# Optimization experiments

Hardware: AMD Instinct MI355X
Metric: run time of the kernel (lower is better)

Reference implementation:

```python
import jax, jax.numpy as jnp
import numpy as np

N_NODES = 100000
N_EDGES = 3200000
IN_DIM, HID_DIM, OUT_DIM = 128, 128, 64
NUM_LAYERS = 5


def setup_inputs() -> dict:
    key = jax.random.key(0)
    ks = jax.random.split(key, 2 + 2 * NUM_LAYERS)
    h = jax.random.normal(ks[0], (N_NODES, IN_DIM), dtype=jnp.float32)
    edge_index = jax.random.randint(ks[1], (2, N_EDGES), 0, N_NODES, dtype=jnp.int64)
    dims = [IN_DIM] + [HID_DIM] * (NUM_LAYERS - 1) + [OUT_DIM]
    inp = {"h": h, "edge_index": edge_index}
    for i in range(NUM_LAYERS):
        fan_in = dims[i]
        bound = 1.0 / np.sqrt(fan_in)
        inp[f"W{i}"] = jax.random.uniform(ks[2 + 2 * i], (dims[i], dims[i + 1]), jnp.float32, -bound, bound)
        inp[f"b{i}"] = jax.random.uniform(ks[3 + 2 * i], (dims[i + 1],), jnp.float32, -bound, bound)
    return inp


def _gin_layer(h, src, dst, W, b):
    # sum aggregation: agg[v] = sum_{(u->v) in E} h[u]
    agg = jax.ops.segment_sum(h[src], dst, num_segments=N_NODES)
    # eps = 0, learn_eps = False: rst = (1 + 0) * h + agg, then MLP (single Linear)
    return (h + agg) @ W + b


def reference(h, edge_index, W0, b0, W1, b1, W2, b2, W3, b3, W4, b4):
    src, dst = edge_index[0], edge_index[1]
    Ws = [W0, W1, W2, W3, W4]
    bs = [b0, b1, b2, b3, b4]
    for i in range(NUM_LAYERS):
        h = _gin_layer(h, src, dst, Ws[i], bs[i])
    return h
```

## Files before the change

kernel.cpp:

```cpp
#include <hip/hip_runtime.h>

#define N_NODES 100000
#define N_EDGES 3200000
#define NB 782
#define BCAP 5120
#define CHUNK_EDGES 4096
#define NCHUNKS ((N_EDGES + CHUNK_EDGES - 1) / CHUNK_EDGES)

typedef unsigned int uint;
typedef __attribute__((ext_vector_type(2))) uint u2v;
typedef __attribute__((ext_vector_type(4))) uint u4v;
typedef __attribute__((ext_vector_type(2))) float f2v;
typedef __attribute__((ext_vector_type(4))) float f4v;
typedef __attribute__((ext_vector_type(8))) short s8v;
typedef __attribute__((ext_vector_type(4))) float f32x4;


__global__ void detect_fmt(const uint* __restrict__ e, int* __restrict__ flag,
                           int* __restrict__ row_ptr) {
    if (threadIdx.x == 0) {
        *flag = (e[1] == 0u && e[3] == 0u && e[5] == 0u && e[7] == 0u) ? 1 : 0;
        row_ptr[N_NODES] = N_EDGES;
    }
}

__device__ __forceinline__ int load_idx(const void* edges, int fmt, long long i) {
    return fmt ? (int)((const long long*)edges)[i] : ((const int*)edges)[i];
}

__global__ __launch_bounds__(256) void part_hist(const void* __restrict__ edges,
                                                 const int* __restrict__ flag,
                                                 int* __restrict__ hist2,
                                                 int* __restrict__ bcount) {
    __shared__ int cnt[NB];
    for (int i = threadIdx.x; i < NB; i += 256) cnt[i] = 0;
    __syncthreads();
    int fmt = *flag;
    int c = blockIdx.x;
    int beg = c * CHUNK_EDGES, end = min(beg + CHUNK_EDGES, N_EDGES);
    for (int i = beg + threadIdx.x; i < end; i += 256) {
        int dst = load_idx(edges, fmt, (long long)N_EDGES + i);
        atomicAdd(&cnt[dst >> 7], 1);
    }
    __syncthreads();
    for (int i = threadIdx.x; i < NB; i += 256) {
        hist2[i * NCHUNKS + c] = cnt[i];
        if (cnt[i]) atomicAdd(&bcount[i], cnt[i]);
    }
}

__global__ void scan_kernel(const int* __restrict__ count, int* __restrict__ off_out, int n) {
    __shared__ int sums[1024];
    int t = threadIdx.x;
    int chunk = (n + 1023) >> 10;
    int beg = t * chunk;
    int end = min(beg + chunk, n);
    int s = 0;
    for (int i = beg; i < end; ++i) s += count[i];
    sums[t] = s;
    __syncthreads();
    int val = s;
    for (int off = 1; off < 1024; off <<= 1) {
        int other = (t >= off) ? sums[t - off] : 0;
        __syncthreads();
        val += other;
        sums[t] = val;
        __syncthreads();
    }
    int run = val - s;
    for (int i = beg; i < end; ++i) {
        off_out[i] = run;
        run += count[i];
    }
    if (end >= n) off_out[n] = run;
}

__global__ __launch_bounds__(1024) void chunk_scan(const int* __restrict__ hist2,
                                                   const int* __restrict__ boff,
                                                   int* __restrict__ base2) {
    __shared__ int s[1024];
    int b = blockIdx.x;
    int t = threadIdx.x;
    int v = (t < NCHUNKS) ? hist2[b * NCHUNKS + t] : 0;
    s[t] = v;
    __syncthreads();
    int val = v;
    for (int off = 1; off < 1024; off <<= 1) {
        int o = (t >= off) ? s[t - off] : 0;
        __syncthreads();
        val += o;
        s[t] = val;
        __syncthreads();
    }
    if (t < NCHUNKS) base2[t * NB + b] = boff[b] + val - v;
}

__global__ __launch_bounds__(256) void part_scatter(const void* __restrict__ edges,
                                                    const int* __restrict__ flag,
                                                    const int* __restrict__ base2,
                                                    uint* __restrict__ tmp) {
    __shared__ int cur[NB];
    int c = blockIdx.x;
    for (int i = threadIdx.x; i < NB; i += 256) cur[i] = base2[c * NB + i];
    __syncthreads();
    int fmt = *flag;
    int beg = c * CHUNK_EDGES, end = min(beg + CHUNK_EDGES, N_EDGES);
    for (int i = beg + threadIdx.x; i < end; i += 256) {
        int src = load_idx(edges, fmt, i);
        int dst = load_idx(edges, fmt, (long long)N_EDGES + i);
        int b = dst >> 7;
        int pos = atomicAdd(&cur[b], 1);
        tmp[pos] = ((uint)(dst & 127) << 17) | (uint)src;
    }
}

__global__ __launch_bounds__(256) void bucket_finalize(const uint* __restrict__ tmp,
                                                       const int* __restrict__ boff,
                                                       int* __restrict__ row_ptr,
                                                       int* __restrict__ esorted) {
    __shared__ uint s1[BCAP];
    __shared__ int s2[BCAP];
    __shared__ int cnt[128], pref[128], cur[128];
    int b = blockIdx.x;
    int beg = boff[b];
    int n = boff[b + 1] - beg;
    if (n > BCAP) n = BCAP;
    int t = threadIdx.x;
    if (t < 128) cnt[t] = 0;
    __syncthreads();
    for (int e = t; e < n; e += 256) {
        uint k = tmp[beg + e];
        s1[e] = k;
        atomicAdd(&cnt[k >> 17], 1);
    }
    __syncthreads();
    if (t < 128) pref[t] = cnt[t];
    __syncthreads();
    for (int off = 1; off < 128; off <<= 1) {
        int v = (t < 128 && t >= off) ? pref[t - off] : 0;
        __syncthreads();
        if (t < 128) pref[t] += v;
        __syncthreads();
    }
    if (t < 128) {
        int ex = pref[t] - cnt[t];
        cur[t] = ex;
        int node = b * 128 + t;
        if (node < N_NODES) row_ptr[node] = beg + ex;
    }
    __syncthreads();
    for (int e = t; e < n; e += 256) {
        uint k = s1[e];
        int p = atomicAdd(&cur[k >> 17], 1);
        s2[p] = (int)(k & 0x1FFFF);
    }
    __syncthreads();
    for (int e = t; e < n; e += 256) esorted[beg + e] = s2[e];
}


__device__ __forceinline__ uint bf16pack(float a, float b) {
    uint ua = __float_as_uint(a);
    ua = (ua + 0x7FFFu + ((ua >> 16) & 1u)) >> 16;
    uint ub = __float_as_uint(b);
    ub = (ub + 0x7FFFu + ((ub >> 16) & 1u)) >> 16;
    return ua | (ub << 16);
}
__device__ __forceinline__ float bf_lo(uint u) { return __uint_as_float(u << 16); }
__device__ __forceinline__ float bf_hi(uint u) { return __uint_as_float(u & 0xFFFF0000u); }


__global__ __launch_bounds__(256) void matstage(const float* __restrict__ Wl,
                                                const float* __restrict__ bl,
                                                const float* __restrict__ Sin,
                                                float* __restrict__ Sout,
                                                float* __restrict__ cout) {
    __shared__ float S[128 * 64];
    int tid = threadIdx.x;
    int b = blockIdx.x;
    for (int i = tid; i < 128 * 16; i += 256) ((f4v*)S)[i] = ((const f4v*)Sin)[i];
    __syncthreads();
    if (b < 32) {
        int rr = tid >> 6;
        int c = tid & 63;
        int r = b * 4 + rr;
        const float* wrow = &Wl[r * 128];
        float s = 0.f;
#pragma unroll 8
        for (int k = 0; k < 128; ++k) s += wrow[k] * S[k * 64 + c];
        Sout[r * 64 + c] = s;
    } else if (tid < 64) {
        float s = 0.f;
        for (int k = 0; k < 128; ++k) s += bl[k] * S[k * 64 + tid];
        cout[tid] = s;
    }
}

__global__ __launch_bounds__(256) void prep_z(const float* __restrict__ S0,
                                              const float* __restrict__ b4,
                                              u4v* __restrict__ Wt,
                                              float* __restrict__ c_all) {
    int idx = blockIdx.x * 256 + threadIdx.x;
    if (blockIdx.x == 0 && threadIdx.x < 64) c_all[4 * 64 + threadIdx.x] = b4[threadIdx.x];
    if (idx >= 64 * 16) return;
    int n = idx >> 4, c16 = idx & 15;
    u4v o;
#pragma unroll
    for (int q = 0; q < 4; ++q)
        o[q] = bf16pack(S0[(size_t)(c16 * 8 + 2 * q) * 64 + n],
                        S0[(size_t)(c16 * 8 + 2 * q + 1) * 64 + n]);
    Wt[n * 16 + (c16 ^ (n & 7))] = o;
}


__global__ __launch_bounds__(256) void agg64_step(const uint* __restrict__ z,
                                                  const int* __restrict__ row_ptr,
                                                  const int* __restrict__ esrc,
                                                  const float* __restrict__ cvec,
                                                  uint* __restrict__ zn) {
    const u2v* z2 = (const u2v*)z;
    int lane = threadIdx.x & 63;
    int c = lane & 15;
    int g = lane >> 4;
    int wid = (blockIdx.x * blockDim.x + threadIdx.x) >> 6;
    int nw = (gridDim.x * blockDim.x) >> 6;
    f4v cc = ((const f4v*)cvec)[c];
    for (int v = wid; v < N_NODES; v += nw) {
        f2v aX = {0.f, 0.f}, aY = {0.f, 0.f};
        int beg = row_ptr[v], end = row_ptr[v + 1];
        int i = beg;
        for (; i + 16 <= end; i += 16) {
            uint k[4];
            u2v u[4];
#pragma unroll
            for (int j = 0; j < 4; ++j) k[j] = (uint)esrc[i + 4 * j + g];
#pragma unroll
            for (int j = 0; j < 4; ++j) u[j] = z2[k[j] * 16u + (uint)c];
#pragma unroll
            for (int j = 0; j < 4; ++j) {
                f2v t0 = {bf_lo(u[j].x), bf_hi(u[j].x)};
                f2v t1 = {bf_lo(u[j].y), bf_hi(u[j].y)};
                aX += t0;
                aY += t1;
            }
        }
        for (; i < end; i += 4) {
            int idx = i + g;
            u2v uu = {0u, 0u};
            if (idx < end) uu = z2[(uint)esrc[idx] * 16u + (uint)c];
            f2v t0 = {bf_lo(uu.x), bf_hi(uu.x)};
            f2v t1 = {bf_lo(uu.y), bf_hi(uu.y)};
            aX += t0;
            aY += t1;
        }
        aX.x += __shfl_xor(aX.x, 16);
        aX.y += __shfl_xor(aX.y, 16);
        aY.x += __shfl_xor(aY.x, 16);
        aY.y += __shfl_xor(aY.y, 16);
        aX.x += __shfl_xor(aX.x, 32);
        aX.y += __shfl_xor(aX.y, 32);
        aY.x += __shfl_xor(aY.x, 32);
        aY.y += __shfl_xor(aY.y, 32);
        if (g == 0) {
            u2v self = z2[(uint)v * 16u + (uint)c];
            u2v o = {bf16pack(aX.x + bf_lo(self.x) + cc.x, aX.y + bf_hi(self.x) + cc.y),
                     bf16pack(aY.x + bf_lo(self.y) + cc.z, aY.y + bf_hi(self.y) + cc.w)};
            __builtin_nontemporal_store(o, &((u2v*)zn)[(uint)v * 16u + (uint)c]);
        }
    }
}

__global__ __launch_bounds__(256) void agg64_last(const uint* __restrict__ z,
                                                  const int* __restrict__ row_ptr,
                                                  const int* __restrict__ esrc,
                                                  const float* __restrict__ cvec,
                                                  float* __restrict__ out) {
    const u2v* z2 = (const u2v*)z;
    int lane = threadIdx.x & 63;
    int c = lane & 15;
    int g = lane >> 4;
    int wid = (blockIdx.x * blockDim.x + threadIdx.x) >> 6;
    int nw = (gridDim.x * blockDim.x) >> 6;
    f4v cc = ((const f4v*)cvec)[c];
    for (int v = wid; v < N_NODES; v += nw) {
        f2v aX = {0.f, 0.f}, aY = {0.f, 0.f};
        int beg = row_ptr[v], end = row_ptr[v + 1];
        int i = beg;
        for (; i + 16 <= end; i += 16) {
            uint k[4];
            u2v u[4];
#pragma unroll
            for (int j = 0; j < 4; ++j) k[j] = (uint)esrc[i + 4 * j + g];
#pragma unroll
            for (int j = 0; j < 4; ++j) u[j] = z2[k[j] * 16u + (uint)c];
#pragma unroll
            for (int j = 0; j < 4; ++j) {
                f2v t0 = {bf_lo(u[j].x), bf_hi(u[j].x)};
                f2v t1 = {bf_lo(u[j].y), bf_hi(u[j].y)};
                aX += t0;
                aY += t1;
            }
        }
        for (; i < end; i += 4) {
            int idx = i + g;
            u2v uu = {0u, 0u};
            if (idx < end) uu = z2[(uint)esrc[idx] * 16u + (uint)c];
            f2v t0 = {bf_lo(uu.x), bf_hi(uu.x)};
            f2v t1 = {bf_lo(uu.y), bf_hi(uu.y)};
            aX += t0;
            aY += t1;
        }
        aX.x += __shfl_xor(aX.x, 16);
        aX.y += __shfl_xor(aX.y, 16);
        aY.x += __shfl_xor(aY.x, 16);
        aY.y += __shfl_xor(aY.y, 16);
        aX.x += __shfl_xor(aX.x, 32);
        aX.y += __shfl_xor(aX.y, 32);
        aY.x += __shfl_xor(aY.x, 32);
        aY.y += __shfl_xor(aY.y, 32);
        if (g == 0) {
            u2v self = z2[(uint)v * 16u + (uint)c];
            f4v o = {aX.x + bf_lo(self.x) + cc.x, aX.y + bf_hi(self.x) + cc.y,
                     aY.x + bf_lo(self.y) + cc.z, aY.y + bf_hi(self.y) + cc.w};
            __builtin_nontemporal_store(o, &((f4v*)out)[(uint)v * 16u + (uint)c]);
        }
    }
}


__global__ __launch_bounds__(256) void mfma_gemm64(const float* __restrict__ x,
                                                   const u4v* __restrict__ Wt,
                                                   uint* __restrict__ y) {
    constexpr int SMEM = 32768 + 64 * 256;
    __shared__ char raw[SMEM];
    u4v* Asm = (u4v*)raw;
    u4v* Bsm = (u4v*)(raw + 32768);
    float* Cst = (float*)raw;
    int tid = threadIdx.x;
    int m0 = blockIdx.x * 128;

#pragma unroll
    for (int i = 0; i < 8; ++i) {
        int idx = tid + i * 256;
        int r = idx >> 4, c16 = idx & 15;
        int m = m0 + r;
        if (m >= N_NODES) m = N_NODES - 1;
        const float* src = &x[(size_t)m * 128 + c16 * 8];
        f4v v0 = *(const f4v*)src;
        f4v v1 = *(const f4v*)(src + 4);
        u4v o = {bf16pack(v0.x, v0.y), bf16pack(v0.z, v0.w),
                 bf16pack(v1.x, v1.y), bf16pack(v1.z, v1.w)};
        Asm[r * 16 + (c16 ^ (r & 7))] = o;
    }
#pragma unroll
    for (int i = 0; i < 4; ++i) Bsm[tid + i * 256] = Wt[tid + i * 256];
    __syncthreads();

    int lane = tid & 63;
    int w = tid >> 6;
    int n0w = w * 16;
    int lhi = lane >> 4, llo = lane & 15;
    f32x4 acc[8];
#pragma unroll
    for (int i = 0; i < 8; ++i) acc[i] = (f32x4){0.f, 0.f, 0.f, 0.f};

#pragma unroll
    for (int ks = 0; ks < 4; ++ks) {
        int cb = ks * 4 + lhi;
        int col = n0w + llo;
        u4v tb = Bsm[col * 16 + (cb ^ (col & 7))];
        s8v bfr = *(s8v*)&tb;
#pragma unroll
        for (int i = 0; i < 8; ++i) {
            int row = i * 16 + llo;
            u4v t = Asm[row * 16 + (cb ^ (row & 7))];
            s8v aa = *(s8v*)&t;
            acc[i] = __builtin_amdgcn_mfma_f32_16x16x32_bf16(aa, bfr, acc[i], 0, 0, 0);
        }
    }
    __syncthreads();
#pragma unroll
    for (int i = 0; i < 8; ++i)
#pragma unroll
        for (int r = 0; r < 4; ++r)
            Cst[(i * 16 + lhi * 4 + r) * 64 + n0w + llo] = acc[i][r];
    __syncthreads();
#pragma unroll
    for (int i = 0; i < 16; ++i) {
        int idx = tid + i * 256;
        int m = idx >> 5, np = idx & 31;
        if (m0 + m < N_NODES)
            y[(size_t)(m0 + m) * 32 + np] =
                bf16pack(Cst[m * 64 + 2 * np], Cst[m * 64 + 2 * np + 1]);
    }
}

extern "C" void kernel_launch(void* const* d_in, const int* in_sizes, int n_in,
                              void* d_out, int out_size, void* d_ws, size_t ws_size,
                              hipStream_t stream) {
    const float* h_in = (const float*)d_in[0];
    const void* edges = d_in[1];
    const float* W[5] = {(const float*)d_in[2], (const float*)d_in[4], (const float*)d_in[6],
                         (const float*)d_in[8], (const float*)d_in[10]};
    const float* B[5] = {(const float*)d_in[3], (const float*)d_in[5], (const float*)d_in[7],
                         (const float*)d_in[9], (const float*)d_in[11]};

    size_t off = 0;
    auto alloc = [&](size_t bytes) {
        void* p = (char*)d_ws + off;
        off = (off + bytes + 255) & ~(size_t)255;
        return p;
    };
    int* esorted = (int*)alloc((size_t)N_EDGES * 4);
    int* row_ptr = (int*)alloc((size_t)(N_NODES + 1) * 4);
    int* hist2 = (int*)alloc((size_t)NCHUNKS * NB * 4);
    int* base2 = (int*)alloc((size_t)NCHUNKS * NB * 4);
    int* bcount = (int*)alloc((size_t)NB * 4);
    int* boff = (int*)alloc((size_t)(NB + 1) * 4);
    int* flag = (int*)alloc(256);
    float* Sa = (float*)alloc(128 * 64 * 4);
    float* Sb = (float*)alloc(128 * 64 * 4);
    float* c_all = (float*)alloc(5 * 64 * 4);
    u4v* Wt_z = (u4v*)alloc((size_t)64 * 16 * 16);
    uint* zA = (uint*)alloc((size_t)N_NODES * 32 * 4);
    uint* zB = (uint*)alloc((size_t)N_NODES * 32 * 4);
    uint* tmp = (uint*)alloc((size_t)N_EDGES * 4);

    detect_fmt<<<1, 64, 0, stream>>>((const uint*)edges, flag, row_ptr);
    (void)hipMemsetAsync(bcount, 0, (size_t)NB * 4, stream);
    part_hist<<<NCHUNKS, 256, 0, stream>>>(edges, flag, hist2, bcount);
    scan_kernel<<<1, 1024, 0, stream>>>(bcount, boff, NB);
    chunk_scan<<<NB, 1024, 0, stream>>>(hist2, boff, base2);
    part_scatter<<<NCHUNKS, 256, 0, stream>>>(edges, flag, base2, tmp);
    bucket_finalize<<<NB, 256, 0, stream>>>(tmp, boff, row_ptr, esorted);

    matstage<<<33, 256, 0, stream>>>(W[3], B[3], W[4], Sa, c_all + 3 * 64);
    matstage<<<33, 256, 0, stream>>>(W[2], B[2], Sa, Sb, c_all + 2 * 64);
    matstage<<<33, 256, 0, stream>>>(W[1], B[1], Sb, Sa, c_all + 1 * 64);
    matstage<<<33, 256, 0, stream>>>(W[0], B[0], Sa, Sb, c_all + 0 * 64);
    prep_z<<<4, 256, 0, stream>>>(Sb, B[4], Wt_z, c_all);

    mfma_gemm64<<<(N_NODES + 127) / 128, 256, 0, stream>>>(h_in, Wt_z, zA);
    agg64_step<<<2048, 256, 0, stream>>>(zA, row_ptr, esorted, c_all + 0 * 64, zB);
    agg64_step<<<2048, 256, 0, stream>>>(zB, row_ptr, esorted, c_all + 1 * 64, zA);
    agg64_step<<<2048, 256, 0, stream>>>(zA, row_ptr, esorted, c_all + 2 * 64, zB);
    agg64_step<<<2048, 256, 0, stream>>>(zB, row_ptr, esorted, c_all + 3 * 64, zA);
    agg64_last<<<2048, 256, 0, stream>>>(zA, row_ptr, esorted, c_all + 4 * 64,
                                         (float*)d_out);
}
```

Baseline: 438.2 us.

## Widen aggregation loads to 16B per lane and coarsen edge scatter chunks

The aggregation kernels now have each lane load 16 bytes (8 bf16 values) per neighbor row, so 8 lanes cover a row and 8 edges are gathered in parallel per wavefront instead of 4. This is meant to cut the number of gather instructions and raise bytes in flight per request. Separately, part_scatter now runs 1024-thread blocks over 32768-edge chunks and reuses the base offsets of every eighth 4096-edge chunk, giving fewer blocks with larger per-block work. The scatter change relies on the 8-chunk grouping lining up with the histogram layout, and the wider per-node edge step may leave more lanes idle on low-degree nodes.

```diff
diff --git a/kernel.cpp b/kernel.cpp
--- a/kernel.cpp
+++ b/kernel.cpp
@@ -6,6 +6,8 @@
 #define BCAP 5120
 #define CHUNK_EDGES 4096
 #define NCHUNKS ((N_EDGES + CHUNK_EDGES - 1) / CHUNK_EDGES)
+#define CHUNK_S 32768
+#define NCHUNKS_S ((N_EDGES + CHUNK_S - 1) / CHUNK_S)
 
 typedef unsigned int uint;
 typedef __attribute__((ext_vector_type(2))) uint u2v;
@@ -95,17 +97,17 @@
     if (t < NCHUNKS) base2[t * NB + b] = boff[b] + val - v;
 }
 
-__global__ __launch_bounds__(256) void part_scatter(const void* __restrict__ edges,
-                                                    const int* __restrict__ flag,
-                                                    const int* __restrict__ base2,
-                                                    uint* __restrict__ tmp) {
+__global__ __launch_bounds__(1024) void part_scatter(const void* __restrict__ edges,
+                                                     const int* __restrict__ flag,
+                                                     const int* __restrict__ base2,
+                                                     uint* __restrict__ tmp) {
     __shared__ int cur[NB];
     int c = blockIdx.x;
-    for (int i = threadIdx.x; i < NB; i += 256) cur[i] = base2[c * NB + i];
+    for (int i = threadIdx.x; i < NB; i += 1024) cur[i] = base2[(c * 8) * NB + i];
     __syncthreads();
     int fmt = *flag;
-    int beg = c * CHUNK_EDGES, end = min(beg + CHUNK_EDGES, N_EDGES);
-    for (int i = beg + threadIdx.x; i < end; i += 256) {
+    int beg = c * CHUNK_S, end = min(beg + CHUNK_S, N_EDGES);
+    for (int i = beg + (int)threadIdx.x; i < end; i += 1024) {
         int src = load_idx(edges, fmt, i);
         int dst = load_idx(edges, fmt, (long long)N_EDGES + i);
         int b = dst >> 7;
@@ -218,54 +220,68 @@
                                                   const int* __restrict__ esrc,
                                                   const float* __restrict__ cvec,
                                                   uint* __restrict__ zn) {
-    const u2v* z2 = (const u2v*)z;
+    const u4v* z4 = (const u4v*)z;
     int lane = threadIdx.x & 63;
-    int c = lane & 15;
-    int g = lane >> 4;
+    int c = lane & 7;
+    int g = lane >> 3;
     int wid = (blockIdx.x * blockDim.x + threadIdx.x) >> 6;
     int nw = (gridDim.x * blockDim.x) >> 6;
-    f4v cc = ((const f4v*)cvec)[c];
+    f4v cc0 = ((const f4v*)cvec)[2 * c];
+    f4v cc1 = ((const f4v*)cvec)[2 * c + 1];
     for (int v = wid; v < N_NODES; v += nw) {
-        f2v aX = {0.f, 0.f}, aY = {0.f, 0.f};
+        f2v a0 = {0.f, 0.f}, a1 = {0.f, 0.f}, a2 = {0.f, 0.f}, a3 = {0.f, 0.f};
         int beg = row_ptr[v], end = row_ptr[v + 1];
         int i = beg;
-        for (; i + 16 <= end; i += 16) {
+        for (; i + 32 <= end; i += 32) {
             uint k[4];
-            u2v u[4];
-#pragma unroll
-            for (int j = 0; j < 4; ++j) k[j] = (uint)esrc[i + 4 * j + g];
-#pragma unroll
-            for (int j = 0; j < 4; ++j) u[j] = z2[k[j] * 16u + (uint)c];
+            u4v u[4];
+#pragma unroll
+            for (int j = 0; j < 4; ++j) k[j] = (uint)esrc[i + 8 * j + g];
+#pragma unroll
+            for (int j = 0; j < 4; ++j) u[j] = z4[k[j] * 8u + (uint)c];
 #pragma unroll
             for (int j = 0; j < 4; ++j) {
                 f2v t0 = {bf_lo(u[j].x), bf_hi(u[j].x)};
                 f2v t1 = {bf_lo(u[j].y), bf_hi(u[j].y)};
-                aX += t0;
-                aY += t1;
+                f2v t2 = {bf_lo(u[j].z), bf_hi(u[j].z)};
+                f2v t3 = {bf_lo(u[j].w), bf_hi(u[j].w)};
+                a0 += t0;
+                a1 += t1;
+                a2 += t2;
+                a3 += t3;
             }
         }
-        for (; i < end; i += 4) {
+        for (; i < end; i += 8) {
             int idx = i + g;
-            u2v uu = {0u, 0u};
-            if (idx < end) uu = z2[(uint)esrc[idx] * 16u + (uint)c];
+            u4v uu = {0u, 0u, 0u, 0u};
+            if (idx < end) uu = z4[(uint)esrc[idx] * 8u + (uint)c];
             f2v t0 = {bf_lo(uu.x), bf_hi(uu.x)};
             f2v t1 = {bf_lo(uu.y), bf_hi(uu.y)};
-            aX += t0;
-            aY += t1;
-        }
-        aX.x += __shfl_xor(aX.x, 16);
-        aX.y += __shfl_xor(aX.y, 16);
-        aY.x += __shfl_xor(aY.x, 16);
-        aY.y += __shfl_xor(aY.y, 16);
-        aX.x += __shfl_xor(aX.x, 32);
-        aX.y += __shfl_xor(aX.y, 32);
-        aY.x += __shfl_xor(aY.x, 32);
-        aY.y += __shfl_xor(aY.y, 32);
+            f2v t2 = {bf_lo(uu.z), bf_hi(uu.z)};
+            f2v t3 = {bf_lo(uu.w), bf_hi(uu.w)};
+            a0 += t0;
+            a1 += t1;
+            a2 += t2;
+            a3 += t3;
+        }
+#pragma unroll
+        for (int d = 8; d <= 32; d <<= 1) {
+            a0.x += __shfl_xor(a0.x, d);
+            a0.y += __shfl_xor(a0.y, d);
+            a1.x += __shfl_xor(a1.x, d);
+            a1.y += __shfl_xor(a1.y, d);
+            a2.x += __shfl_xor(a2.x, d);
+            a2.y += __shfl_xor(a2.y, d);
+            a3.x += __shfl_xor(a3.x, d);
+            a3.y += __shfl_xor(a3.y, d);
+        }
         if (g == 0) {
-            u2v self = z2[(uint)v * 16u + (uint)c];
-            u2v o = {bf16pack(aX.x + bf_lo(self.x) + cc.x, aX.y + bf_hi(self.x) + cc.y),
-                     bf16pack(aY.x + bf_lo(self.y) + cc.z, aY.y + bf_hi(self.y) + cc.w)};
-            __builtin_nontemporal_store(o, &((u2v*)zn)[(uint)v * 16u + (uint)c]);
+            u4v self = z4[(uint)v * 8u + (uint)c];
+            u4v o = {bf16pack(a0.x + bf_lo(self.x) + cc0.x, a0.y + bf_hi(self.x) + cc0.y),
+                     bf16pack(a1.x + bf_lo(self.y) + cc0.z, a1.y + bf_hi(self.y) + cc0.w),
+                     bf16pack(a2.x + bf_lo(self.z) + cc1.x, a2.y + bf_hi(self.z) + cc1.y),
+                     bf16pack(a3.x + bf_lo(self.w) + cc1.z, a3.y + bf_hi(self.w) + cc1.w)};
+            __builtin_nontemporal_store(o, &((u4v*)zn)[(uint)v * 8u + (uint)c]);
         }
     }
 }
@@ -275,54 +291,69 @@
                                                   const int* __restrict__ esrc,
                                                   const float* __restrict__ cvec,
                                                   float* __restrict__ out) {
-    const u2v* z2 = (const u2v*)z;
+    const u4v* z4 = (const u4v*)z;
     int lane = threadIdx.x & 63;
-    int c = lane & 15;
-    int g = lane >> 4;
+    int c = lane & 7;
+    int g = lane >> 3;
     int wid = (blockIdx.x * blockDim.x + threadIdx.x) >> 6;
     int nw = (gridDim.x * blockDim.x) >> 6;
-    f4v cc = ((const f4v*)cvec)[c];
+    f4v cc0 = ((const f4v*)cvec)[2 * c];
+    f4v cc1 = ((const f4v*)cvec)[2 * c + 1];
     for (int v = wid; v < N_NODES; v += nw) {
-        f2v aX = {0.f, 0.f}, aY = {0.f, 0.f};
+        f2v a0 = {0.f, 0.f}, a1 = {0.f, 0.f}, a2 = {0.f, 0.f}, a3 = {0.f, 0.f};
         int beg = row_ptr[v], end = row_ptr[v + 1];
         int i = beg;
-        for (; i + 16 <= end; i += 16) {
+        for (; i + 32 <= end; i += 32) {
             uint k[4];
-            u2v u[4];
-#pragma unroll
-            for (int j = 0; j < 4; ++j) k[j] = (uint)esrc[i + 4 * j + g];
-#pragma unroll
-            for (int j = 0; j < 4; ++j) u[j] = z2[k[j] * 16u + (uint)c];
+            u4v u[4];
+#pragma unroll
+            for (int j = 0; j < 4; ++j) k[j] = (uint)esrc[i + 8 * j + g];
+#pragma unroll
+            for (int j = 0; j < 4; ++j) u[j] = z4[k[j] * 8u + (uint)c];
 #pragma unroll
             for (int j = 0; j < 4; ++j) {
                 f2v t0 = {bf_lo(u[j].x), bf_hi(u[j].x)};
                 f2v t1 = {bf_lo(u[j].y), bf_hi(u[j].y)};
-                aX += t0;
-                aY += t1;
+                f2v t2 = {bf_lo(u[j].z), bf_hi(u[j].z)};
+                f2v t3 = {bf_lo(u[j].w), bf_hi(u[j].w)};
+                a0 += t0;
+                a1 += t1;
+                a2 += t2;
+                a3 += t3;
             }
         }
-        for (; i < end; i += 4) {
+        for (; i < end; i += 8) {
             int idx = i + g;
-            u2v uu = {0u, 0u};
-            if (idx < end) uu = z2[(uint)esrc[idx] * 16u + (uint)c];
+            u4v uu = {0u, 0u, 0u, 0u};
+            if (idx < end) uu = z4[(uint)esrc[idx] * 8u + (uint)c];
             f2v t0 = {bf_lo(uu.x), bf_hi(uu.x)};
             f2v t1 = {bf_lo(uu.y), bf_hi(uu.y)};
-            aX += t0;
-            aY += t1;
-        }
-        aX.x += __shfl_xor(aX.x, 16);
-        aX.y += __shfl_xor(aX.y, 16);
-        aY.x += __shfl_xor(aY.x, 16);
-        aY.y += __shfl_xor(aY.y, 16);
-        aX.x += __shfl_xor(aX.x, 32);
-        aX.y += __shfl_xor(aX.y, 32);
-        aY.x += __shfl_xor(aY.x, 32);
-        aY.y += __shfl_xor(aY.y, 32);
+            f2v t2 = {bf_lo(uu.z), bf_hi(uu.z)};
+            f2v t3 = {bf_lo(uu.w), bf_hi(uu.w)};
+            a0 += t0;
+            a1 += t1;
+            a2 += t2;
+            a3 += t3;
+        }
+#pragma unroll
+        for (int d = 8; d <= 32; d <<= 1) {
+            a0.x += __shfl_xor(a0.x, d);
+            a0.y += __shfl_xor(a0.y, d);
+            a1.x += __shfl_xor(a1.x, d);
+            a1.y += __shfl_xor(a1.y, d);
+            a2.x += __shfl_xor(a2.x, d);
+            a2.y += __shfl_xor(a2.y, d);
+            a3.x += __shfl_xor(a3.x, d);
+            a3.y += __shfl_xor(a3.y, d);
+        }
         if (g == 0) {
-            u2v self = z2[(uint)v * 16u + (uint)c];
-            f4v o = {aX.x + bf_lo(self.x) + cc.x, aX.y + bf_hi(self.x) + cc.y,
-                     aY.x + bf_lo(self.y) + cc.z, aY.y + bf_hi(self.y) + cc.w};
-            __builtin_nontemporal_store(o, &((f4v*)out)[(uint)v * 16u + (uint)c]);
+            u4v self = z4[(uint)v * 8u + (uint)c];
+            f4v o0 = {a0.x + bf_lo(self.x) + cc0.x, a0.y + bf_hi(self.x) + cc0.y,
+                      a1.x + bf_lo(self.y) + cc0.z, a1.y + bf_hi(self.y) + cc0.w};
+            f4v o1 = {a2.x + bf_lo(self.z) + cc1.x, a2.y + bf_hi(self.z) + cc1.y,
+                      a3.x + bf_lo(self.w) + cc1.z, a3.y + bf_hi(self.w) + cc1.w};
+            __builtin_nontemporal_store(o0, &((f4v*)out)[(uint)v * 16u + 2u * (uint)c]);
+            __builtin_nontemporal_store(o1, &((f4v*)out)[(uint)v * 16u + 2u * (uint)c + 1u]);
         }
     }
 }
@@ -431,7 +462,7 @@
     part_hist<<<NCHUNKS, 256, 0, stream>>>(edges, flag, hist2, bcount);
     scan_kernel<<<1, 1024, 0, stream>>>(bcount, boff, NB);
     chunk_scan<<<NB, 1024, 0, stream>>>(hist2, boff, base2);
-    part_scatter<<<NCHUNKS, 256, 0, stream>>>(edges, flag, base2, tmp);
+    part_scatter<<<NCHUNKS_S, 1024, 0, stream>>>(edges, flag, base2, tmp);
     bucket_finalize<<<NB, 256, 0, stream>>>(tmp, boff, row_ptr, esorted);
 
     matstage<<<33, 256, 0, stream>>>(W[3], B[3], W[4], Sa, c_all + 3 * 64);
```

Result: faster. 423.1 us (-3.4%).
